# Performance work log

Measured on AMD Instinct MI355X. Metric: run time of the kernel, lower is better.

The kernel has to match this reference:

```python
import jax, jax.numpy as jnp
import numpy as np

ALPHA = 1.5
EPS = 1e-5
N_BISECT = 30

BSZ, NFIELD, NFEAT, NEMB, DK, NHID, MLP_NHID, NOUT = 2048, 100, 100000, 64, 64, 256, 1024, 1


def _entmax_bisect(x):
    """alpha-entmax (alpha=1.5) along last axis via bisection on tau."""
    x = x * (ALPHA - 1.0)
    mx = jnp.max(x, axis=-1, keepdims=True)
    d = x.shape[-1]
    tau_lo = mx - 1.0
    tau_hi = mx - (1.0 / d) ** (ALPHA - 1.0)
    inv_am1 = 1.0 / (ALPHA - 1.0)  # = 2.0 for alpha=1.5

    def p_of(tau):
        return jnp.maximum(x - tau, 0.0) ** inv_am1

    dm0 = tau_hi - tau_lo

    def body(i, carry):
        tau_lo, dm = carry
        dm = dm * 0.5
        tau_m = tau_lo + dm
        f_m = jnp.sum(p_of(tau_m), axis=-1, keepdims=True) - 1.0
        tau_lo = jnp.where(f_m >= 0, tau_m, tau_lo)
        return (tau_lo, dm)

    tau_lo, dm = jax.lax.fori_loop(0, N_BISECT, body, (tau_lo, dm0))
    p = p_of(tau_lo)
    return p / jnp.sum(p, axis=-1, keepdims=True)


@jax.custom_vjp
def entmax(x):
    return _entmax_bisect(x)

def _entmax_fwd(x):
    p = _entmax_bisect(x)
    return p, p

def _entmax_bwd(p, g):
    # exact entmax jacobian-vector product (as in entmax library)
    gppr = jnp.where(p > 0, p ** (2.0 - ALPHA), 0.0)
    dx = g * gppr
    q = jnp.sum(dx, axis=-1, keepdims=True) / jnp.sum(gppr, axis=-1, keepdims=True)
    return (dx - q * gppr,)

entmax.defvjp(_entmax_fwd, _entmax_bwd)


def _bn(x, gamma, beta, axes, ch_shape):
    mean = jnp.mean(x, axis=axes, keepdims=True)
    var = jnp.var(x, axis=axes, keepdims=True)
    return gamma.reshape(ch_shape) * (x - mean) / jnp.sqrt(var + EPS) + beta.reshape(ch_shape)


def setup_inputs() -> dict:
    key = jax.random.key(0)
    ks = jax.random.split(key, 12)
    inp = {
        "ids": jax.random.randint(ks[0], (BSZ, NFIELD), 0, NFEAT),
        "values": jax.random.uniform(ks[1], (BSZ, NFIELD), dtype=jnp.float32),
        "emb_table": jax.random.normal(ks[2], (NFEAT, NEMB), dtype=jnp.float32) * 0.01,
        "w_bilinear": jax.random.normal(ks[3], (DK, NEMB), dtype=jnp.float32) * (1.0 / np.sqrt(NEMB)),
        "query": jax.random.normal(ks[4], (NHID, DK), dtype=jnp.float32) * (1.414 / np.sqrt(NHID + DK)),
        "att_values": jax.random.normal(ks[5], (NHID, NFIELD), dtype=jnp.float32) * 0.01,
        "bn_gamma": jnp.ones((NHID,), jnp.float32),
        "bn_beta": jnp.zeros((NHID,), jnp.float32),
        "mlp_w0": jax.random.normal(ks[6], (MLP_NHID, NHID * NEMB), dtype=jnp.float32) * (1.0 / np.sqrt(NHID * NEMB)),
        "mlp_b0": jnp.zeros((MLP_NHID,), jnp.float32),
        "mlp_g0": jnp.ones((MLP_NHID,), jnp.float32),
        "mlp_be0": jnp.zeros((MLP_NHID,), jnp.float32),
        "mlp_w1": jax.random.normal(ks[7], (MLP_NHID, MLP_NHID), dtype=jnp.float32) * (1.0 / np.sqrt(MLP_NHID)),
        "mlp_b1": jnp.zeros((MLP_NHID,), jnp.float32),
        "mlp_g1": jnp.ones((MLP_NHID,), jnp.float32),
        "mlp_be1": jnp.zeros((MLP_NHID,), jnp.float32),
        "out_w": jax.random.normal(ks[8], (NOUT, MLP_NHID), dtype=jnp.float32) * (1.0 / np.sqrt(MLP_NHID)),
        "out_b": jnp.zeros((NOUT,), jnp.float32),
    }
    return inp


def reference(ids, values, emb_table, w_bilinear, query, att_values, bn_gamma, bn_beta,
              mlp_w0, mlp_b0, mlp_g0, mlp_be0, mlp_w1, mlp_b1, mlp_g1, mlp_be1, out_w, out_b):
    v = jnp.clip(values, 0.001, 1.0)                        # [b,f]
    emb = emb_table[ids] * v[..., None]                     # [b,f,e]
    keys = jnp.einsum('bfe,ke->bfk', emb, w_bilinear)       # [b,f,dk]
    gates = jnp.einsum('bfk,ok->bof', keys, query) * (DK ** -0.5)  # [b,o,f]
    sparse_gates = entmax(gates)                            # [b,o,f]
    arm_w = sparse_gates * att_values[None]                 # [b,o,f]
    arm = jnp.exp(jnp.einsum('bfe,bof->boe', emb, arm_w))   # [b,o,e]
    arm = _bn(arm, bn_gamma, bn_beta, axes=(0, 2), ch_shape=(1, -1, 1))
    h = arm.reshape(arm.shape[0], -1)                       # [b, o*e]
    h = jax.nn.relu(_bn(h @ mlp_w0.T + mlp_b0, mlp_g0, mlp_be0, axes=(0,), ch_shape=(1, -1)))
    h = jax.nn.relu(_bn(h @ mlp_w1.T + mlp_b1, mlp_g1, mlp_be1, axes=(0,), ch_shape=(1, -1)))
    y = h @ out_w.T + out_b                                 # [b,1]
    return y.squeeze(-1)
```

## Files before the change

kernel.cpp:

```cpp
#include <hip/hip_runtime.h>

typedef unsigned short u16;
typedef __attribute__((ext_vector_type(8))) short bf16x8;
typedef __attribute__((ext_vector_type(8))) unsigned short u16x8;
typedef __attribute__((ext_vector_type(4))) float f32x4;

__device__ __forceinline__ u16 f2bf(float f) {
  unsigned u = __builtin_bit_cast(unsigned, f);
  u += 0x7fffu + ((u >> 16) & 1u);
  return (u16)(u >> 16);
}
__device__ __forceinline__ float bf2f(u16 h) {
  unsigned u = ((unsigned)h) << 16;
  return __builtin_bit_cast(float, u);
}

#define NB 2048
#define NF 100
#define NE 64
#define NO 256
#define OCH 64
#define EMB_ST 72
#define EMBT_ST 136
#define GAW_ST 136

#define GLOAD16(gsrc, ldst)                                                        \
  __builtin_amdgcn_global_load_lds(                                                \
      (const __attribute__((address_space(1))) unsigned int*)(gsrc),               \
      (__attribute__((address_space(3))) unsigned int*)(ldst), 16, 0, 0)

__global__ void k_prep_M(const float* __restrict__ wb, const float* __restrict__ q,
                         u16* __restrict__ mt) {
  int idx = blockIdx.x * 256 + threadIdx.x;
  int o = idx >> 6, e = idx & 63;
  float s = 0.f;
  for (int k = 0; k < 64; ++k) s = fmaf(q[o * 64 + k], wb[k * 64 + e], s);
  mt[idx] = f2bf(s * 0.0625f);
}

__global__ void k_cvt(const float* __restrict__ in, u16* __restrict__ out, int n) {
  int i4 = (blockIdx.x * 256 + threadIdx.x) * 4;
  if (i4 >= n) return;
  float4 v = *(const float4*)(in + i4);
  ushort4 o;
  o.x = f2bf(v.x); o.y = f2bf(v.y); o.z = f2bf(v.z); o.w = f2bf(v.w);
  *(ushort4*)(out + i4) = o;
}

__global__ void k_cvt_w0s(const float* __restrict__ in, const float* __restrict__ scl,
                          u16* __restrict__ out) {
  size_t i4 = ((size_t)blockIdx.x * 256 + threadIdx.x) * 4;
  int o = (int)((i4 >> 6) & 255);
  float sc = scl[o];
  float4 v = *(const float4*)(in + i4);
  ushort4 u;
  u.x = f2bf(v.x * sc); u.y = f2bf(v.y * sc);
  u.z = f2bf(v.z * sc); u.w = f2bf(v.w * sc);
  *(ushort4*)(out + i4) = u;
}

__global__ __launch_bounds__(256) void k_mega(
    const int* __restrict__ ids, const float* __restrict__ vals,
    const float* __restrict__ etab, const u16* __restrict__ mt,
    const float* __restrict__ att, u16* __restrict__ tbuf) {
  __shared__ u16 s_emb[112][EMB_ST];
  __shared__ u16 s_embT[64][EMBT_ST];
  __shared__ u16 s_gaw[64][GAW_ST];
  __shared__ float s_rs[64];

  const int tid = threadIdx.x;
  const int lane = tid & 63;
  const int wid = tid >> 6;
  const int b = blockIdx.x;

  for (int f = wid; f < NF; f += 4) {
    int id = ids[b * NF + f];
    float v = vals[b * NF + f];
    v = fminf(fmaxf(v, 0.001f), 1.0f);
    float ev = etab[(size_t)id * NE + lane] * v;
    u16 bf = f2bf(ev);
    s_emb[f][lane] = bf;
    s_embT[lane][f] = bf;
  }
  for (int i = tid; i < 12 * EMB_ST; i += 256) s_emb[100 + i / EMB_ST][i % EMB_ST] = 0;
  for (int i = tid; i < 64 * 36; i += 256) s_embT[i / 36][100 + i % 36] = 0;
  for (int i = tid; i < 64 * 24; i += 256) s_gaw[i / 24][112 + i % 24] = 0;
  __syncthreads();

  for (int oc = 0; oc < 4; ++oc) {
    const int obase = oc * OCH;
    bf16x8 amt[2];
#pragma unroll
    for (int kh = 0; kh < 2; ++kh)
      amt[kh] = *(const bf16x8*)(mt + ((obase + wid * 16 + (lane & 15)) * 64 +
                                       kh * 32 + ((lane >> 4) * 8)));

#pragma unroll
    for (int ft = 0; ft < 7; ++ft) {
      f32x4 acc = {0.f, 0.f, 0.f, 0.f};
#pragma unroll
      for (int kh = 0; kh < 2; ++kh) {
        bf16x8 bfr = *(const bf16x8*)&s_emb[ft * 16 + (lane & 15)][kh * 32 + ((lane >> 4) * 8)];
        acc = __builtin_amdgcn_mfma_f32_16x16x32_bf16(amt[kh], bfr, acc, 0, 0, 0);
      }
      int fc = ft * 16 + (lane & 15);
      if (fc < NF) {
#pragma unroll
        for (int i = 0; i < 4; ++i)
          s_gaw[wid * 16 + ((lane >> 4) * 4) + i][fc] = f2bf(acc[i]);
      }
    }
    __syncthreads();

    {
      const int q = tid & 3;
      const int r = tid >> 2;
      const int og = obase + r;
      float x[28];
#pragma unroll
      for (int j = 0; j < 7; ++j) {
        ushort4 g = *(const ushort4*)&s_gaw[r][j * 16 + q * 4];
        x[j * 4 + 0] = bf2f(g.x); x[j * 4 + 1] = bf2f(g.y);
        x[j * 4 + 2] = bf2f(g.z); x[j * 4 + 3] = bf2f(g.w);
      }
      if (q > 0) { x[24] = -1e30f; x[25] = -1e30f; x[26] = -1e30f; x[27] = -1e30f; }
      float attv[28];
#pragma unroll
      for (int j = 0; j < 7; ++j) {
        if (j < 6 || q == 0) {
          float4 av = *(const float4*)(att + og * NF + j * 16 + q * 4);
          attv[j * 4 + 0] = av.x; attv[j * 4 + 1] = av.y;
          attv[j * 4 + 2] = av.z; attv[j * 4 + 3] = av.w;
        } else {
          attv[j * 4 + 0] = 0.f; attv[j * 4 + 1] = 0.f;
          attv[j * 4 + 2] = 0.f; attv[j * 4 + 3] = 0.f;
        }
      }
      float m0 = x[0], m1 = x[1];
#pragma unroll
      for (int j = 2; j < 28; j += 2) { m0 = fmaxf(m0, x[j]); m1 = fmaxf(m1, x[j + 1]); }
      float mx = fmaxf(m0, m1);
      mx = fmaxf(mx, __shfl_xor(mx, 1));
      mx = fmaxf(mx, __shfl_xor(mx, 2));
      float tau = mx - 1.0f;
#pragma unroll
      for (int it = 0; it < 6; ++it) {
        float s0 = 0.f, s1 = 0.f, t0 = 0.f, t1 = 0.f;
#pragma unroll
        for (int j = 0; j < 14; ++j) {
          float d0 = fmaxf(x[j] - tau, 0.f);
          float d1 = fmaxf(x[j + 14] - tau, 0.f);
          s0 = fmaf(d0, d0, s0); s1 = fmaf(d1, d1, s1);
          t0 += d0; t1 += d1;
        }
        float s = s0 + s1, sd = t0 + t1;
        s += __shfl_xor(s, 1);
        s += __shfl_xor(s, 2);
        sd += __shfl_xor(sd, 1);
        sd += __shfl_xor(sd, 2);
        tau += (s - 1.0f) / (2.0f * sd + 1e-30f);
      }
      float s0 = 0.f, s1 = 0.f;
#pragma unroll
      for (int j = 0; j < 14; ++j) {
        float d0 = fmaxf(x[j] - tau, 0.f);
        float d1 = fmaxf(x[j + 14] - tau, 0.f);
        x[j] = d0 * d0;
        x[j + 14] = d1 * d1;
        s0 += x[j]; s1 += x[j + 14];
      }
      float s = s0 + s1;
      s += __shfl_xor(s, 1);
      s += __shfl_xor(s, 2);
      if (q == 0) s_rs[r] = 1.0f / s;
#pragma unroll
      for (int j = 0; j < 7; ++j) {
        ushort4 w;
        w.x = f2bf(x[j * 4 + 0] * attv[j * 4 + 0]);
        w.y = f2bf(x[j * 4 + 1] * attv[j * 4 + 1]);
        w.z = f2bf(x[j * 4 + 2] * attv[j * 4 + 2]);
        w.w = f2bf(x[j * 4 + 3] * attv[j * 4 + 3]);
        *(ushort4*)&s_gaw[r][j * 16 + q * 4] = w;
      }
    }
    __syncthreads();

    f32x4 acc[4] = {};
#pragma unroll
    for (int h = 0; h < 4; ++h) {
      bf16x8 afr = *(const bf16x8*)&s_gaw[wid * 16 + (lane & 15)][h * 32 + ((lane >> 4) * 8)];
#pragma unroll
      for (int et = 0; et < 4; ++et) {
        bf16x8 bfr = *(const bf16x8*)&s_embT[et * 16 + (lane & 15)][h * 32 + ((lane >> 4) * 8)];
        acc[et] = __builtin_amdgcn_mfma_f32_16x16x32_bf16(afr, bfr, acc[et], 0, 0, 0);
      }
    }
    const int rbase = wid * 16 + ((lane >> 4) * 4);
    float rs4[4];
#pragma unroll
    for (int i = 0; i < 4; ++i) rs4[i] = s_rs[rbase + i];
    size_t orow = (size_t)b * NO + obase + rbase;
#pragma unroll
    for (int et = 0; et < 4; ++et) {
      int e = et * 16 + (lane & 15);
#pragma unroll
      for (int i = 0; i < 4; ++i)
        tbuf[(orow + i) * 64 + e] = f2bf(__expf(acc[et][i] * rs4[i]) - 1.0f);
    }
    __syncthreads();
  }
}

__global__ void k_stats_o_part(const u16* __restrict__ t, float* __restrict__ pstat) {
  const int o = blockIdx.x, bs = blockIdx.y;
  const int e = threadIdx.x & 63, bt = threadIdx.x >> 6;
  float s = 0.f, s2 = 0.f;
  for (int b = bs * 256 + bt; b < bs * 256 + 256; b += 4) {
    float v = bf2f(t[((size_t)b * NO + o) * 64 + e]);
    s += v;
    s2 = fmaf(v, v, s2);
  }
  __shared__ float red[2][256];
  red[0][threadIdx.x] = s; red[1][threadIdx.x] = s2;
  __syncthreads();
  for (int st = 128; st >= 1; st >>= 1) {
    if (threadIdx.x < st) {
      red[0][threadIdx.x] += red[0][threadIdx.x + st];
      red[1][threadIdx.x] += red[1][threadIdx.x + st];
    }
    __syncthreads();
  }
  if (threadIdx.x == 0) {
    pstat[((size_t)bs * NO + o) * 2] = red[0][0];
    pstat[((size_t)bs * NO + o) * 2 + 1] = red[1][0];
  }
}

__global__ void k_stats_o_fin(const float* __restrict__ pstat, const float* __restrict__ g,
                              float* __restrict__ scl) {
  int o = threadIdx.x;
  float s = 0.f, s2 = 0.f;
#pragma unroll
  for (int p = 0; p < 8; ++p) {
    s  += pstat[((size_t)p * NO + o) * 2];
    s2 += pstat[((size_t)p * NO + o) * 2 + 1];
  }
  float invN = 1.0f / (float)(NB * 64);
  float m = s * invN;
  float var = s2 * invN - m * m;
  scl[o] = g[o] * rsqrtf(var + 1e-5f);
}

__global__ __launch_bounds__(256) void k_gemm(const u16* __restrict__ A,
                                              const u16* __restrict__ B,
                                              float* __restrict__ C,
                                              int M, int N, int K, int ksz) {
  __shared__ u16 sA[128][64];
  __shared__ u16 sB[128][64];
  const int tid = threadIdx.x, lane = tid & 63, wid = tid >> 6;
  const int wr = wid >> 1, wc = wid & 1;
  const int m0 = blockIdx.x * 128, n0 = blockIdx.y * 128;
  const int k0 = blockIdx.z * ksz;
  C += (size_t)blockIdx.z * ((size_t)M * N);
  f32x4 acc[4][4];
#pragma unroll
  for (int mi = 0; mi < 4; ++mi)
#pragma unroll
    for (int ni = 0; ni < 4; ++ni) acc[mi][ni] = (f32x4){0.f, 0.f, 0.f, 0.f};

  const int lrow = lane >> 3;
  const int lch = lane & 7;
  const u16* gA = A + (size_t)(m0 + wid * 32 + lrow) * K + k0 + lch * 8;
  const u16* gB = B + (size_t)(n0 + wid * 32 + lrow) * K + k0 + lch * 8;
  u16* lA = &sA[wid * 32][0];
  u16* lB = &sB[wid * 32][0];

  const int nkt = ksz / 64;
  for (int kt = 0; kt < nkt; ++kt) {
#pragma unroll
    for (int i = 0; i < 4; ++i) {
      GLOAD16(gA + (size_t)i * 8 * K, lA + i * 512);
      GLOAD16(gB + (size_t)i * 8 * K, lB + i * 512);
    }
    gA += 64; gB += 64;
    __syncthreads();
#pragma unroll
    for (int kh = 0; kh < 2; ++kh) {
      bf16x8 af[4], bfv[4];
#pragma unroll
      for (int i = 0; i < 4; ++i) {
        af[i]  = *(const bf16x8*)&sA[wr * 64 + i * 16 + (lane & 15)][kh * 32 + ((lane >> 4) * 8)];
        bfv[i] = *(const bf16x8*)&sB[wc * 64 + i * 16 + (lane & 15)][kh * 32 + ((lane >> 4) * 8)];
      }
#pragma unroll
      for (int mi = 0; mi < 4; ++mi)
#pragma unroll
        for (int ni = 0; ni < 4; ++ni)
          acc[mi][ni] = __builtin_amdgcn_mfma_f32_16x16x32_bf16(af[mi], bfv[ni], acc[mi][ni], 0, 0, 0);
    }
    __syncthreads();
  }
#pragma unroll
  for (int mi = 0; mi < 4; ++mi) {
    int m = m0 + wr * 64 + mi * 16 + ((lane >> 4) * 4);
#pragma unroll
    for (int ni = 0; ni < 4; ++ni) {
      int n = n0 + wc * 64 + ni * 16 + (lane & 15);
#pragma unroll
      for (int i = 0; i < 4; ++i) C[(size_t)(m + i) * N + n] = acc[mi][ni][i];
    }
  }
}

template <int NP>
__global__ void k_red_stats(const float* __restrict__ c, float* __restrict__ r,
                            float* __restrict__ pstat) {
  const int col = blockIdx.x * 64 + (threadIdx.x & 63);
  const int rt = threadIdx.x >> 6;
  const int rg = blockIdx.y;
  const size_t ps = (size_t)NB * 1024;
  float s = 0.f, s2 = 0.f;
  for (int rr = rt; rr < 64; rr += 4) {
    size_t idx = (size_t)(rg * 64 + rr) * 1024 + col;
    float v = c[idx];
#pragma unroll
    for (int p = 1; p < NP; ++p) v += c[p * ps + idx];
    r[idx] = v;
    s += v;
    s2 = fmaf(v, v, s2);
  }
  __shared__ float red[2][256];
  red[0][threadIdx.x] = s; red[1][threadIdx.x] = s2;
  __syncthreads();
  if (threadIdx.x < 64) {
    int t = threadIdx.x;
    s  = red[0][t] + red[0][t + 64] + red[0][t + 128] + red[0][t + 192];
    s2 = red[1][t] + red[1][t + 64] + red[1][t + 128] + red[1][t + 192];
    pstat[((size_t)rg * 1024 + col) * 2]     = s;
    pstat[((size_t)rg * 1024 + col) * 2 + 1] = s2;
  }
}

__global__ void k_stats_fin(const float* __restrict__ pstat,
                            const float* __restrict__ g, const float* __restrict__ be,
                            float* __restrict__ scl, float* __restrict__ bia) {
  int col = blockIdx.x * 256 + threadIdx.x;
  float s = 0.f, s2 = 0.f;
#pragma unroll
  for (int p = 0; p < 32; ++p) {
    s  += pstat[((size_t)p * 1024 + col) * 2];
    s2 += pstat[((size_t)p * 1024 + col) * 2 + 1];
  }
  float invN = 1.0f / (float)NB;
  float m = s * invN;
  float var = s2 * invN - m * m;
  float inv = rsqrtf(var + 1e-5f);
  scl[col] = g[col] * inv;
  bia[col] = be[col] - g[col] * inv * m;
}

__global__ void k_applyA1(const float* __restrict__ c0,
                          const float* __restrict__ scl, const float* __restrict__ bia,
                          u16* __restrict__ a1) {
  size_t i4 = ((size_t)blockIdx.x * 256 + threadIdx.x) * 4;
  int n = (int)(i4 & 1023);
  float4 v0 = *(const float4*)(c0 + i4);
  ushort4 o;
  o.x = f2bf(fmaxf(fmaf(v0.x, scl[n + 0], bia[n + 0]), 0.f));
  o.y = f2bf(fmaxf(fmaf(v0.y, scl[n + 1], bia[n + 1]), 0.f));
  o.z = f2bf(fmaxf(fmaf(v0.z, scl[n + 2], bia[n + 2]), 0.f));
  o.w = f2bf(fmaxf(fmaf(v0.w, scl[n + 3], bia[n + 3]), 0.f));
  *(ushort4*)(a1 + i4) = o;
}

__global__ void k_final(const float* __restrict__ h, const float* __restrict__ scl,
                        const float* __restrict__ bia, const float* __restrict__ ow,
                        const float* __restrict__ ob, float* __restrict__ y) {
  int lane = threadIdx.x & 63, wid = threadIdx.x >> 6;
  int row = blockIdx.x * 4 + wid;
  const float* hr = h + (size_t)row * 1024;
  float part = 0.f;
#pragma unroll
  for (int j = 0; j < 16; ++j) {
    int n = j * 64 + lane;
    float v = fmaxf(fmaf(hr[n], scl[n], bia[n]), 0.f);
    part = fmaf(v, ow[n], part);
  }
#pragma unroll
  for (int off = 32; off >= 1; off >>= 1) part += __shfl_xor(part, off);
  if (lane == 0) y[row] = part + ob[0];
}

extern "C" void kernel_launch(void* const* d_in, const int* in_sizes, int n_in,
                              void* d_out, int out_size, void* d_ws, size_t ws_size,
                              hipStream_t stream) {
  const int*   ids   = (const int*)d_in[0];
  const float* vals  = (const float*)d_in[1];
  const float* etab  = (const float*)d_in[2];
  const float* wb    = (const float*)d_in[3];
  const float* query = (const float*)d_in[4];
  const float* att   = (const float*)d_in[5];
  const float* bng   = (const float*)d_in[6];
  const float* w0    = (const float*)d_in[8];
  const float* g0    = (const float*)d_in[10];
  const float* be0   = (const float*)d_in[11];
  const float* w1    = (const float*)d_in[12];
  const float* g1    = (const float*)d_in[14];
  const float* be1   = (const float*)d_in[15];
  const float* outw  = (const float*)d_in[16];
  const float* outb  = (const float*)d_in[17];
  float* y = (float*)d_out;

  char* ws = (char*)d_ws;
  u16*   mt     = (u16*)(ws + 0);
  u16*   w0bf   = (u16*)(ws + 32768ull);
  u16*   w1bf   = (u16*)(ws + 33587200ull);
  u16*   tbuf   = (u16*)(ws + 35684352ull);
  float* c01    = (float*)(ws + 102793216ull);
  float* h1     = (float*)(ws + 102793216ull);
  float* r0     = (float*)(ws + 169902080ull);
  u16*   a1     = (u16*)(ws + 178290688ull);
  float* h      = (float*)(ws + 186679296ull);
  float* pstat1 = (float*)(ws + 195067904ull);
  float* pstat2 = (float*)(ws + 195330048ull);
  float* pstatO = (float*)(ws + 195592192ull);
  float* sclA   = (float*)(ws + 195608576ull);
  float* scl1   = (float*)(ws + 195609600ull);
  float* bia1   = (float*)(ws + 195613696ull);
  float* scl2   = (float*)(ws + 195617792ull);
  float* bia2   = (float*)(ws + 195621888ull);

  k_prep_M<<<64, 256, 0, stream>>>(wb, query, mt);
  k_cvt<<<1024, 256, 0, stream>>>(w1, w1bf, 1024 * 1024);
  k_mega<<<2048, 256, 0, stream>>>(ids, vals, etab, mt, att, tbuf);
  k_stats_o_part<<<dim3(256, 8), 256, 0, stream>>>(tbuf, pstatO);
  k_stats_o_fin<<<1, 256, 0, stream>>>(pstatO, bng, sclA);
  k_cvt_w0s<<<16384, 256, 0, stream>>>(w0, sclA, w0bf);
  k_gemm<<<dim3(16, 8, 8), 256, 0, stream>>>(tbuf, w0bf, c01, 2048, 1024, 16384, 2048);
  k_red_stats<8><<<dim3(16, 32), 256, 0, stream>>>(c01, r0, pstat1);
  k_stats_fin<<<4, 256, 0, stream>>>(pstat1, g0, be0, scl1, bia1);
  k_applyA1<<<2048, 256, 0, stream>>>(r0, scl1, bia1, a1);
  k_gemm<<<dim3(16, 8, 4), 256, 0, stream>>>(a1, w1bf, h1, 2048, 1024, 1024, 256);
  k_red_stats<4><<<dim3(16, 32), 256, 0, stream>>>(h1, h, pstat2);
  k_stats_fin<<<4, 256, 0, stream>>>(pstat2, g1, be1, scl2, bia2);
  k_final<<<512, 256, 0, stream>>>(h, scl2, bia2, outw, outb, y);
}
```

Baseline: 290.1 us.

## Pipeline GEMM with triple-buffered LDS prefetch and halve split-K factor

Replaces the synchronous GEMM with a version that keeps a 3-stage ring of 32-wide K tiles in LDS, issuing global-to-LDS loads three tiles ahead. Two waves load A and two load B, and MFMA runs at raised priority between the barriers. The split-K factors are halved for both MLP GEMMs, which shrinks the partial-sum buffers and the reduction work in k_red_stats. In exchange there are fewer blocks in flight and a longer serial K loop per block, plus more LDS per block.

```diff
diff --git a/kernel.cpp b/kernel.cpp
--- a/kernel.cpp
+++ b/kernel.cpp
@@ -251,55 +251,74 @@
   scl[o] = g[o] * rsqrtf(var + 1e-5f);
 }
 
-__global__ __launch_bounds__(256) void k_gemm(const u16* __restrict__ A,
-                                              const u16* __restrict__ B,
-                                              float* __restrict__ C,
-                                              int M, int N, int K, int ksz) {
-  __shared__ u16 sA[128][64];
-  __shared__ u16 sB[128][64];
+__global__ __launch_bounds__(256) void k_gemmp(const u16* __restrict__ A,
+                                               const u16* __restrict__ B,
+                                               float* __restrict__ C,
+                                               int M, int N, int K, int ksz) {
+  __shared__ u16 lds[3 * 8192];
   const int tid = threadIdx.x, lane = tid & 63, wid = tid >> 6;
   const int wr = wid >> 1, wc = wid & 1;
   const int m0 = blockIdx.x * 128, n0 = blockIdx.y * 128;
   const int k0 = blockIdx.z * ksz;
   C += (size_t)blockIdx.z * ((size_t)M * N);
+
   f32x4 acc[4][4];
 #pragma unroll
   for (int mi = 0; mi < 4; ++mi)
 #pragma unroll
     for (int ni = 0; ni < 4; ++ni) acc[mi][ni] = (f32x4){0.f, 0.f, 0.f, 0.f};
 
-  const int lrow = lane >> 3;
-  const int lch = lane & 7;
-  const u16* gA = A + (size_t)(m0 + wid * 32 + lrow) * K + k0 + lch * 8;
-  const u16* gB = B + (size_t)(n0 + wid * 32 + lrow) * K + k0 + lch * 8;
-  u16* lA = &sA[wid * 32][0];
-  u16* lB = &sB[wid * 32][0];
-
-  const int nkt = ksz / 64;
-  for (int kt = 0; kt < nkt; ++kt) {
+  const u16* gstage = (wid < 2)
+      ? A + (size_t)(m0 + wid * 64 + (lane >> 2)) * K + k0 + (lane & 3) * 8
+      : B + (size_t)(n0 + (wid - 2) * 64 + (lane >> 2)) * K + k0 + (lane & 3) * 8;
+  const int lstage = (wid < 2) ? (wid * 64) * 32 : 4096 + ((wid - 2) * 64) * 32;
+
+  const int la15 = lane & 15, la4 = lane >> 4;
+  const u16* aoff = lds + (wr * 64 + la15) * 32 + la4 * 8;
+  const u16* boff = lds + 4096 + (wc * 64 + la15) * 32 + la4 * 8;
+
+  const int nkt = ksz / 32;
+#pragma unroll
+  for (int t = 0; t < 3; ++t)
+#pragma unroll
+    for (int i = 0; i < 4; ++i)
+      GLOAD16(gstage + (size_t)t * 32 + (size_t)i * 16 * K, lds + t * 8192 + lstage + i * 512);
+  asm volatile("s_waitcnt vmcnt(8)" ::: "memory");
+  __builtin_amdgcn_sched_barrier(0);
+  __builtin_amdgcn_s_barrier();
+  __builtin_amdgcn_sched_barrier(0);
+
+  int slot = 0;
+  for (int j = 0; j < nkt; ++j) {
+    bf16x8 af[4], bfv[4];
 #pragma unroll
     for (int i = 0; i < 4; ++i) {
-      GLOAD16(gA + (size_t)i * 8 * K, lA + i * 512);
-      GLOAD16(gB + (size_t)i * 8 * K, lB + i * 512);
-    }
-    gA += 64; gB += 64;
-    __syncthreads();
-#pragma unroll
-    for (int kh = 0; kh < 2; ++kh) {
-      bf16x8 af[4], bfv[4];
-#pragma unroll
-      for (int i = 0; i < 4; ++i) {
-        af[i]  = *(const bf16x8*)&sA[wr * 64 + i * 16 + (lane & 15)][kh * 32 + ((lane >> 4) * 8)];
-        bfv[i] = *(const bf16x8*)&sB[wc * 64 + i * 16 + (lane & 15)][kh * 32 + ((lane >> 4) * 8)];
-      }
-#pragma unroll
-      for (int mi = 0; mi < 4; ++mi)
-#pragma unroll
-        for (int ni = 0; ni < 4; ++ni)
-          acc[mi][ni] = __builtin_amdgcn_mfma_f32_16x16x32_bf16(af[mi], bfv[ni], acc[mi][ni], 0, 0, 0);
-    }
-    __syncthreads();
-  }
+      af[i]  = *(const bf16x8*)(aoff + slot * 8192 + i * 512);
+      bfv[i] = *(const bf16x8*)(boff + slot * 8192 + i * 512);
+    }
+    asm volatile("s_waitcnt lgkmcnt(0)" ::: "memory");
+    __builtin_amdgcn_sched_barrier(0);
+    __builtin_amdgcn_s_barrier();
+    __builtin_amdgcn_sched_barrier(0);
+    const int ts = (j + 3 < nkt) ? j + 3 : nkt - 1;
+#pragma unroll
+    for (int i = 0; i < 4; ++i)
+      GLOAD16(gstage + (size_t)ts * 32 + (size_t)i * 16 * K,
+              lds + slot * 8192 + lstage + i * 512);
+    __builtin_amdgcn_s_setprio(1);
+#pragma unroll
+    for (int mi = 0; mi < 4; ++mi)
+#pragma unroll
+      for (int ni = 0; ni < 4; ++ni)
+        acc[mi][ni] = __builtin_amdgcn_mfma_f32_16x16x32_bf16(af[mi], bfv[ni], acc[mi][ni], 0, 0, 0);
+    __builtin_amdgcn_s_setprio(0);
+    asm volatile("s_waitcnt vmcnt(8)" ::: "memory");
+    __builtin_amdgcn_sched_barrier(0);
+    __builtin_amdgcn_s_barrier();
+    __builtin_amdgcn_sched_barrier(0);
+    slot = (slot == 2) ? 0 : slot + 1;
+  }
+
 #pragma unroll
   for (int mi = 0; mi < 4; ++mi) {
     int m = m0 + wr * 64 + mi * 16 + ((lane >> 4) * 4);
@@ -436,12 +455,12 @@
   k_stats_o_part<<<dim3(256, 8), 256, 0, stream>>>(tbuf, pstatO);
   k_stats_o_fin<<<1, 256, 0, stream>>>(pstatO, bng, sclA);
   k_cvt_w0s<<<16384, 256, 0, stream>>>(w0, sclA, w0bf);
-  k_gemm<<<dim3(16, 8, 8), 256, 0, stream>>>(tbuf, w0bf, c01, 2048, 1024, 16384, 2048);
-  k_red_stats<8><<<dim3(16, 32), 256, 0, stream>>>(c01, r0, pstat1);
+  k_gemmp<<<dim3(16, 8, 4), 256, 0, stream>>>(tbuf, w0bf, c01, 2048, 1024, 16384, 4096);
+  k_red_stats<4><<<dim3(16, 32), 256, 0, stream>>>(c01, r0, pstat1);
   k_stats_fin<<<4, 256, 0, stream>>>(pstat1, g0, be0, scl1, bia1);
   k_applyA1<<<2048, 256, 0, stream>>>(r0, scl1, bia1, a1);
-  k_gemm<<<dim3(16, 8, 4), 256, 0, stream>>>(a1, w1bf, h1, 2048, 1024, 1024, 256);
-  k_red_stats<4><<<dim3(16, 32), 256, 0, stream>>>(h1, h, pstat2);
+  k_gemmp<<<dim3(16, 8, 2), 256, 0, stream>>>(a1, w1bf, h1, 2048, 1024, 1024, 512);
+  k_red_stats<2><<<dim3(16, 32), 256, 0, stream>>>(h1, h, pstat2);
   k_stats_fin<<<4, 256, 0, stream>>>(pstat2, g1, be1, scl2, bia2);
   k_final<<<512, 256, 0, stream>>>(h, scl2, bia2, outw, outb, y);
 }
```

After: 273.9 us. 1.06x faster.
